# Kernel tuning notes

Measured on AMD Instinct MI355X. Metric: run time of the kernel, lower is better.

Reference implementation:

```python
import jax, jax.numpy as jnp
import numpy as np

EMBED_DIM = 1024
NUM_HEADS = 16
HEAD_DIM = EMBED_DIM // NUM_HEADS
B, S = 4, 1024
EPS = 1e-5
NEG = -1e9


def layer_norm(h, gamma, beta):
    mu = jnp.mean(h, axis=-1, keepdims=True)
    var = jnp.mean(jnp.square(h - mu), axis=-1, keepdims=True)
    return (h - mu) * jax.lax.rsqrt(var + EPS) * gamma + beta


def setup_inputs() -> dict:
    key = jax.random.key(0)
    ks = jax.random.split(key, 8)
    scale = 1.0 / np.sqrt(EMBED_DIM)
    x = jax.random.normal(ks[0], (B, S, EMBED_DIM), dtype=jnp.float32)
    mask = jax.random.randint(ks[1], (B, S, S), 0, 2).astype(jnp.bool_)
    Wq = jax.random.uniform(ks[2], (EMBED_DIM, EMBED_DIM), jnp.float32, -scale, scale)
    bq = jax.random.uniform(ks[3], (EMBED_DIM,), jnp.float32, -scale, scale)
    Wk = jax.random.uniform(ks[4], (EMBED_DIM, EMBED_DIM), jnp.float32, -scale, scale)
    bk = jax.random.uniform(ks[5], (EMBED_DIM,), jnp.float32, -scale, scale)
    gq = jnp.ones((EMBED_DIM,), jnp.float32)
    bq_n = jnp.zeros((EMBED_DIM,), jnp.float32)
    gk = jnp.ones((EMBED_DIM,), jnp.float32)
    bk_n = jnp.zeros((EMBED_DIM,), jnp.float32)
    return {"x": x, "mask": mask, "Wq": Wq, "bq": bq, "Wk": Wk, "bk": bk,
            "gq": gq, "bq_n": bq_n, "gk": gk, "bk_n": bk_n}


def reference(x, mask, Wq, bq, Wk, bk, gq, bq_n, gk, bk_n):
    b, s, _ = x.shape
    # proj -> LayerNorm -> ReLU, split heads: [B,S,H,D]
    Q = jax.nn.relu(layer_norm(x @ Wq + bq, gq, bq_n)).reshape(b, s, NUM_HEADS, HEAD_DIM)
    K = jax.nn.relu(layer_norm(x @ Wk + bk, gk, bk_n)).reshape(b, s, NUM_HEADS, HEAD_DIM)
    # scores [B,H,S,S]
    scores = jnp.einsum('bqhd,bkhd->bhqk', Q, K) / np.sqrt(HEAD_DIM).astype(np.float32)
    # symmetric masking: mask applied along keys, then (via transpose trick) along queries
    m = (mask | jnp.swapaxes(mask, -1, -2))[:, None, :, :]
    scores = jnp.where(m, NEG, scores)
    attn = jax.nn.softmax(scores, axis=-1)
    return attn.mean(axis=1)  # [B,S,S]
```

## Files before the change

kernel.cpp:

```cpp
#include <hip/hip_runtime.h>
#include <hip/hip_bf16.h>

#define B_ 4
#define S_ 1024
#define E_ 1024
#define H_ 16
#define D_ 64

typedef __attribute__((ext_vector_type(8))) short short8;
typedef __attribute__((ext_vector_type(4))) float f32x4;

static __device__ __forceinline__ unsigned short f2bf(float x) {
  unsigned int u = __float_as_uint(x);
  unsigned int r = u + 0x7fffu + ((u >> 16) & 1u);
  return (unsigned short)(r >> 16);
}
static __device__ __forceinline__ float bf2f(unsigned short b) {
  return __uint_as_float((unsigned int)b << 16);
}

#define GL2LDS16(g, l)                                                            \
  __builtin_amdgcn_global_load_lds(                                               \
      (const __attribute__((address_space(1))) unsigned int*)(g),                 \
      (__attribute__((address_space(3))) unsigned int*)(l), 16, 0, 0)

__global__ __launch_bounds__(256) void prep_kernel(const int* __restrict__ mask,
                                                   const float* __restrict__ x,
                                                   const float* __restrict__ Wq,
                                                   const float* __restrict__ Wk,
                                                   unsigned char* __restrict__ msym,
                                                   unsigned short* __restrict__ xbf,
                                                   unsigned short* __restrict__ Wt) {
  __shared__ __align__(16) char u_lds[32 * 33 * 4];
  const int blk = blockIdx.x;
  const int tid = threadIdx.x;
  if (blk < 4096) {
    int (*T)[33] = (int(*)[33])u_lds;
    const int b = blk >> 10;
    const int rest = blk & 1023;
    const int i0 = (rest >> 5) << 5;
    const int j0 = (rest & 31) << 5;
    const int ii = tid >> 3;
    const int jj4 = (tid & 7) << 2;
    const size_t bO = (size_t)b * S_ * S_;
    const int4 m2 = *(const int4*)&mask[bO + (size_t)(j0 + ii) * S_ + i0 + jj4];
    T[ii][jj4 + 0] = m2.x; T[ii][jj4 + 1] = m2.y; T[ii][jj4 + 2] = m2.z; T[ii][jj4 + 3] = m2.w;
    __syncthreads();
    const int4 m1 = *(const int4*)&mask[bO + (size_t)(i0 + ii) * S_ + j0 + jj4];
    uchar4 o;
    o.x = ((m1.x != 0) || (T[jj4 + 0][ii] != 0)) ? 1 : 0;
    o.y = ((m1.y != 0) || (T[jj4 + 1][ii] != 0)) ? 1 : 0;
    o.z = ((m1.z != 0) || (T[jj4 + 2][ii] != 0)) ? 1 : 0;
    o.w = ((m1.w != 0) || (T[jj4 + 3][ii] != 0)) ? 1 : 0;
    *(uchar4*)&msym[bO + (size_t)(i0 + ii) * S_ + j0 + jj4] = o;
  } else if (blk < 6144) {
    const size_t i = ((size_t)(blk - 4096) * 256 + tid) * 8;
    const float4 a = *(const float4*)(x + i);
    const float4 b = *(const float4*)(x + i + 4);
    const ushort4 p0 = {f2bf(a.x), f2bf(a.y), f2bf(a.z), f2bf(a.w)};
    const ushort4 p1 = {f2bf(b.x), f2bf(b.y), f2bf(b.z), f2bf(b.w)};
    *(ushort4*)(xbf + i) = p0;
    *(ushort4*)(xbf + i + 4) = p1;
  } else {
    unsigned short (*T2)[36] = (unsigned short(*)[36])u_lds;
    const int wblk = blk - 6144;
    const int mat = wblk >> 10;
    const int kt = (wblk >> 5) & 31, ntb = wblk & 31;
    const float* W = mat ? Wk : Wq;
    const int r = tid >> 3, c4 = (tid & 7) << 2;
    const float4 v = *(const float4*)&W[(size_t)(kt * 32 + r) * 1024 + ntb * 32 + c4];
    T2[r][c4 + 0] = f2bf(v.x); T2[r][c4 + 1] = f2bf(v.y);
    T2[r][c4 + 2] = f2bf(v.z); T2[r][c4 + 3] = f2bf(v.w);
    __syncthreads();
    const ushort4 o = {T2[c4 + 0][r], T2[c4 + 1][r], T2[c4 + 2][r], T2[c4 + 3][r]};
    *(ushort4*)&Wt[(size_t)(mat * 1024 + ntb * 32 + r) * 1024 + kt * 32 + c4] = o;
  }
}

__global__ __launch_bounds__(256) void gemm_mfma_kernel(const unsigned short* __restrict__ Abf,
                                                        const unsigned short* __restrict__ Wt,
                                                        unsigned short* __restrict__ P,
                                                        int nstride) {
  __shared__ __align__(16) unsigned short As[128 * 64];
  __shared__ __align__(16) unsigned short Bs[128 * 64];
  const int tid = threadIdx.x;
  const int m0 = (blockIdx.x & 31) << 7;
  const int n0 = (blockIdx.x >> 5) << 7;
  const int wave = tid >> 6, lane = tid & 63;
  const int ln15 = lane & 15, rg = lane >> 4;
  const int wm = (wave & 1) << 6;
  const int wn = (wave >> 1) << 6;
  const int sr = tid >> 3;
  const int sc = (tid & 7) << 3;
  const unsigned short* gA = Abf + (size_t)(m0 + sr) * 1024 + sc;
  const unsigned short* gB = Wt + (size_t)(n0 + sr) * 1024 + sc;
  unsigned short* lA = As + tid * 8;
  unsigned short* lB = Bs + tid * 8;
  f32x4 acc[4][4];
#pragma unroll
  for (int i = 0; i < 4; ++i)
#pragma unroll
    for (int j = 0; j < 4; ++j) acc[i][j] = (f32x4){0.0f, 0.0f, 0.0f, 0.0f};

  const unsigned short* pa = As + (wm + ln15) * 64 + rg * 8;
  const unsigned short* pb = Bs + (wn + ln15) * 64 + rg * 8;
  for (int k0 = 0; k0 < E_; k0 += 64) {
#pragma unroll
    for (int j = 0; j < 4; ++j) {
      GL2LDS16(gA + k0 + (size_t)(j * 32) * 1024, lA + j * 2048);
      GL2LDS16(gB + k0 + (size_t)(j * 32) * 1024, lB + j * 2048);
    }
    __syncthreads();
#pragma unroll
    for (int kk = 0; kk < 2; ++kk) {
      short8 af[4], bfr[4];
#pragma unroll
      for (int i = 0; i < 4; ++i) af[i] = *(const short8*)(pa + i * 16 * 64 + kk * 32);
#pragma unroll
      for (int j = 0; j < 4; ++j) bfr[j] = *(const short8*)(pb + j * 16 * 64 + kk * 32);
#pragma unroll
      for (int i = 0; i < 4; ++i)
#pragma unroll
        for (int j = 0; j < 4; ++j)
          acc[i][j] = __builtin_amdgcn_mfma_f32_16x16x32_bf16(af[i], bfr[j], acc[i][j], 0, 0, 0);
    }
    __syncthreads();
  }
#pragma unroll
  for (int i = 0; i < 4; ++i)
#pragma unroll
    for (int j = 0; j < 4; ++j)
#pragma unroll
      for (int r = 0; r < 4; ++r) {
        const int row = m0 + wm + i * 16 + rg * 4 + r;
        const int col = n0 + wn + j * 16 + ln15;
        P[(size_t)row * nstride + col] = f2bf(acc[i][j][r]);
      }
}

__global__ __launch_bounds__(256) void ln_relu_bf_kernel(const unsigned short* __restrict__ P,
                                                         int rowstride, int coloff,
                                                         const float* __restrict__ bias,
                                                         const float* __restrict__ gamma,
                                                         const float* __restrict__ beta,
                                                         unsigned short* __restrict__ obf) {
  const int row = blockIdx.x;
  const int b = row >> 10, s = row & 1023;
  const unsigned short* p = P + (size_t)row * rowstride + coloff;
  const int tid = threadIdx.x;
  const ushort4 pv = *(const ushort4*)(p + tid * 4);
  float4 v = {bf2f(pv.x), bf2f(pv.y), bf2f(pv.z), bf2f(pv.w)};
  const float4 bb = ((const float4*)bias)[tid];
  v.x += bb.x; v.y += bb.y; v.z += bb.z; v.w += bb.w;
  float sum = v.x + v.y + v.z + v.w;
  float s2 = v.x * v.x + v.y * v.y + v.z * v.z + v.w * v.w;
#pragma unroll
  for (int off = 32; off >= 1; off >>= 1) {
    sum += __shfl_xor(sum, off);
    s2 += __shfl_xor(s2, off);
  }
  __shared__ float red[2][4];
  const int wave = tid >> 6, lane = tid & 63;
  if (lane == 0) { red[0][wave] = sum; red[1][wave] = s2; }
  __syncthreads();
  sum = red[0][0] + red[0][1] + red[0][2] + red[0][3];
  s2 = red[1][0] + red[1][1] + red[1][2] + red[1][3];
  const float mu = sum * (1.0f / E_);
  const float var = s2 * (1.0f / E_) - mu * mu;
  const float r = rsqrtf(var + 1e-5f);
  const float4 g = ((const float4*)gamma)[tid];
  const float4 bt = ((const float4*)beta)[tid];
  const float o0 = fmaxf((v.x - mu) * r * g.x + bt.x, 0.0f);
  const float o1 = fmaxf((v.y - mu) * r * g.y + bt.y, 0.0f);
  const float o2 = fmaxf((v.z - mu) * r * g.z + bt.z, 0.0f);
  const float o3 = fmaxf((v.w - mu) * r * g.w + bt.w, 0.0f);
  const int h = tid >> 4;
  const int d = (tid & 15) << 2;
  const ushort4 ob = {f2bf(o0), f2bf(o1), f2bf(o2), f2bf(o3)};
  *(ushort4*)&obf[((size_t)(b * H_ + h) * S_ + s) * D_ + d] = ob;
}

__global__ __launch_bounds__(1024, 4) void attn5_kernel(const unsigned short* __restrict__ Qbf,
                                                        const unsigned short* __restrict__ Kbf,
                                                        const unsigned char* __restrict__ msym,
                                                        float* __restrict__ out) {
  __shared__ __align__(16) unsigned short Qs[256 * 64];
  __shared__ __align__(16) unsigned short Ks[2][256 * 64];
  __shared__ __align__(16) float l_lds[16][16];
  __shared__ __align__(16) float linv[16];
  const int tid = threadIdx.x;
  const int wave = tid >> 6, lane = tid & 63;
  const int ln15 = lane & 15, rg = lane >> 4;
  const int b = blockIdx.x & 3;
  const int q0 = (blockIdx.x >> 2) << 4;

  const unsigned short* Kb = Kbf + (size_t)b * H_ * S_ * D_;

  {
    const int rho = tid >> 3, p = tid & 7;
    const int c = p ^ (rho & 7);
    const int rho2 = rho + 128;
    const int c2 = p ^ (rho2 & 7);
    const uint4 v0 = *(const uint4*)(Qbf + ((size_t)(b * H_ + (rho >> 4)) * S_ + q0 + (rho & 15)) * D_ + c * 8);
    const uint4 v1 = *(const uint4*)(Qbf + ((size_t)(b * H_ + (rho2 >> 4)) * S_ + q0 + (rho2 & 15)) * D_ + c2 * 8);
    *(uint4*)&Qs[rho * 64 + p * 8] = v0;
    *(uint4*)&Qs[rho2 * 64 + p * 8] = v1;
  }
  unsigned int mbits = 0;
#pragma unroll
  for (int qt = 0; qt < 4; ++qt)
#pragma unroll
    for (int r = 0; r < 4; ++r)
      mbits |= (msym[((size_t)b * S_ + q0 + rg * 4 + r) * S_ + qt * 256 + wave * 16 + ln15] ? 1u : 0u)
               << (qt * 4 + r);

  const int krow = tid >> 3, kp = tid & 7;
  const int kcc = kp ^ (krow & 7);
  {
    const unsigned short* src = Kb + (size_t)krow * D_ + kcc * 8;
    const uint4 p0 = *(const uint4*)src;
    const uint4 p1 = *(const uint4*)(src + 128 * D_);
    *(uint4*)&Ks[0][krow * 64 + kp * 8] = p0;
    *(uint4*)&Ks[0][(krow + 128) * 64 + kp * 8] = p1;
  }
  __syncthreads();

  const int pfrag = (rg ^ (ln15 & 7)) * 8;
  const unsigned short* QsW = Qs + ln15 * 64;
  const unsigned short* KsW0 = Ks[0] + (wave * 16 + ln15) * 64;
  const unsigned short* KsW1 = Ks[1] + (wave * 16 + ln15) * 64;

  float o[4][4] = {};
  float ef[4][4];
  uint4 pf0, pf1;

#pragma unroll 1
  for (int h = 0; h < 16; ++h) {
    const unsigned short* qrow = QsW + h * 16 * 64;
    const short8 a0 = *(const short8*)(qrow + pfrag);
    const short8 a1 = *(const short8*)(qrow + (pfrag ^ 32));
    float la[4] = {0.0f, 0.0f, 0.0f, 0.0f};
#pragma unroll
    for (int qt = 0; qt < 4; ++qt) {
      const int s = h * 4 + qt;
      if (s < 63) {
        const int s1 = s + 1;
        const unsigned short* src =
            Kb + ((size_t)(s1 >> 2) * S_ + ((s1 & 3) << 8) + krow) * D_ + kcc * 8;
        pf0 = *(const uint4*)src;
        pf1 = *(const uint4*)(src + 128 * D_);
      }
      const unsigned short* kw = (qt & 1) ? KsW1 : KsW0;
      const short8 b0 = *(const short8*)(kw + pfrag);
      const short8 b1 = *(const short8*)(kw + (pfrag ^ 32));
      f32x4 cc = {0.0f, 0.0f, 0.0f, 0.0f};
      cc = __builtin_amdgcn_mfma_f32_16x16x32_bf16(a0, b0, cc, 0, 0, 0);
      cc = __builtin_amdgcn_mfma_f32_16x16x32_bf16(a1, b1, cc, 0, 0, 0);
#pragma unroll
      for (int r = 0; r < 4; ++r) {
        const float sv = fminf(cc[r] * 0.125f, 80.0f);
        const float ev = ((mbits >> (qt * 4 + r)) & 1u) ? 0.0f : __expf(sv);
        ef[qt][r] = ev;
        la[r] += ev;
      }
      if (s < 63) {
        unsigned short* dst = (qt & 1) ? Ks[0] : Ks[1];
        *(uint4*)&dst[krow * 64 + kp * 8] = pf0;
        *(uint4*)&dst[(krow + 128) * 64 + kp * 8] = pf1;
      }
      if (qt < 3) __syncthreads();
    }
#pragma unroll
    for (int r = 0; r < 4; ++r) {
      float lv = la[r];
      lv += __shfl_xor(lv, 1);
      lv += __shfl_xor(lv, 2);
      lv += __shfl_xor(lv, 4);
      lv += __shfl_xor(lv, 8);
      la[r] = lv;
    }
    if (ln15 == 0) *(float4*)&l_lds[wave][rg * 4] = (float4){la[0], la[1], la[2], la[3]};
    __syncthreads();
    if (tid < 16) {
      float ssum = 0.0f;
#pragma unroll
      for (int w = 0; w < 16; ++w) ssum += l_lds[w][tid];
      linv[tid] = 0.0625f / ssum;
    }
    __syncthreads();
    const float4 li4 = *(const float4*)&linv[rg * 4];
#pragma unroll
    for (int qt = 0; qt < 4; ++qt) {
      o[qt][0] += ef[qt][0] * li4.x;
      o[qt][1] += ef[qt][1] * li4.y;
      o[qt][2] += ef[qt][2] * li4.z;
      o[qt][3] += ef[qt][3] * li4.w;
    }
  }
#pragma unroll
  for (int qt = 0; qt < 4; ++qt)
#pragma unroll
    for (int r = 0; r < 4; ++r)
      out[((size_t)b * S_ + q0 + rg * 4 + r) * S_ + qt * 256 + wave * 16 + ln15] = o[qt][r];
}

extern "C" void kernel_launch(void* const* d_in, const int* in_sizes, int n_in,
                              void* d_out, int out_size, void* d_ws, size_t ws_size,
                              hipStream_t stream) {
  const float* x = (const float*)d_in[0];
  const int* mask = (const int*)d_in[1];
  const float* Wq = (const float*)d_in[2];
  const float* bq = (const float*)d_in[3];
  const float* Wk = (const float*)d_in[4];
  const float* bk = (const float*)d_in[5];
  const float* gq = (const float*)d_in[6];
  const float* bq_n = (const float*)d_in[7];
  const float* gk = (const float*)d_in[8];
  const float* bk_n = (const float*)d_in[9];
  float* out = (float*)d_out;

  char* ws = (char*)d_ws;
  const size_t MB = 1024 * 1024;

  if (ws_size >= 40 * MB) {
    unsigned short* P2 = (unsigned short*)ws;
    unsigned short* xbf = (unsigned short*)(ws + 16 * MB);
    unsigned short* Kbf = (unsigned short*)(ws + 16 * MB);
    unsigned short* Wt = (unsigned short*)(ws + 24 * MB);
    unsigned short* Qbf = (unsigned short*)(ws + 28 * MB);
    unsigned char* msym = (unsigned char*)(ws + 36 * MB);

    prep_kernel<<<8192, 256, 0, stream>>>(mask, x, Wq, Wk, msym, xbf, Wt);
    gemm_mfma_kernel<<<512, 256, 0, stream>>>(xbf, Wt, P2, 2048);
    ln_relu_bf_kernel<<<4096, 256, 0, stream>>>(P2, 2048, 0, bq, gq, bq_n, Qbf);
    ln_relu_bf_kernel<<<4096, 256, 0, stream>>>(P2, 2048, 1024, bk, gk, bk_n, Kbf);
    attn5_kernel<<<256, 1024, 0, stream>>>(Qbf, Kbf, msym, out);
  } else {
    unsigned short* P = (unsigned short*)ws;
    unsigned short* xbf = (unsigned short*)(ws + 8 * MB);
    unsigned short* Kbf = (unsigned short*)(ws + 8 * MB);
    unsigned short* Wt = (unsigned short*)(ws + 16 * MB);
    unsigned short* Qbf = (unsigned short*)(ws + 20 * MB);
    unsigned char* msym = (unsigned char*)(ws + 28 * MB);

    prep_kernel<<<8192, 256, 0, stream>>>(mask, x, Wq, Wk, msym, xbf, Wt);
    gemm_mfma_kernel<<<256, 256, 0, stream>>>(xbf, Wt, P, 1024);
    ln_relu_bf_kernel<<<4096, 256, 0, stream>>>(P, 1024, 0, bq, gq, bq_n, Qbf);
    gemm_mfma_kernel<<<256, 256, 0, stream>>>(xbf, Wt + (size_t)1024 * 1024, P, 1024);
    ln_relu_bf_kernel<<<4096, 256, 0, stream>>>(P, 1024, 0, bk, gk, bk_n, Kbf);
    attn5_kernel<<<256, 1024, 0, stream>>>(Qbf, Kbf, msym, out);
  }
}
```

Before: 199.1 us.

## Stream K tiles via direct global-to-LDS loads in larger halves, merge LN launches

The attention kernel now copies K tiles straight from global memory into LDS (global_load_lds) in 512-key halves instead of 256-key quarters staged through registers. This cuts the barriers per head from four to two and removes register staging. Q fragments are read directly from global memory rather than staged in LDS, and the two LayerNorm launches are merged into one 8192-block kernel. LDS use grows to two 64 KB buffers, which may reduce occupancy.

```diff
diff --git a/kernel.cpp b/kernel.cpp
--- a/kernel.cpp
+++ b/kernel.cpp
@@ -138,16 +138,9 @@
       }
 }
 
-__global__ __launch_bounds__(256) void ln_relu_bf_kernel(const unsigned short* __restrict__ P,
-                                                         int rowstride, int coloff,
-                                                         const float* __restrict__ bias,
-                                                         const float* __restrict__ gamma,
-                                                         const float* __restrict__ beta,
-                                                         unsigned short* __restrict__ obf) {
-  const int row = blockIdx.x;
-  const int b = row >> 10, s = row & 1023;
-  const unsigned short* p = P + (size_t)row * rowstride + coloff;
-  const int tid = threadIdx.x;
+__device__ __forceinline__ void ln_body(const unsigned short* p, const float* bias,
+                                        const float* gamma, const float* beta,
+                                        unsigned short* obf, int b, int s, int tid) {
   const ushort4 pv = *(const ushort4*)(p + tid * 4);
   float4 v = {bf2f(pv.x), bf2f(pv.y), bf2f(pv.z), bf2f(pv.w)};
   const float4 bb = ((const float4*)bias)[tid];
@@ -180,12 +173,39 @@
   *(ushort4*)&obf[((size_t)(b * H_ + h) * S_ + s) * D_ + d] = ob;
 }
 
-__global__ __launch_bounds__(1024, 4) void attn5_kernel(const unsigned short* __restrict__ Qbf,
+__global__ __launch_bounds__(256) void ln_relu_bf_kernel(const unsigned short* __restrict__ P,
+                                                         int rowstride, int coloff,
+                                                         const float* __restrict__ bias,
+                                                         const float* __restrict__ gamma,
+                                                         const float* __restrict__ beta,
+                                                         unsigned short* __restrict__ obf) {
+  const int row = blockIdx.x;
+  ln_body(P + (size_t)row * rowstride + coloff, bias, gamma, beta, obf,
+          row >> 10, row & 1023, threadIdx.x);
+}
+
+__global__ __launch_bounds__(256) void ln2_kernel(const unsigned short* __restrict__ P2,
+                                                  const float* __restrict__ bq,
+                                                  const float* __restrict__ gq,
+                                                  const float* __restrict__ bqn,
+                                                  const float* __restrict__ bk,
+                                                  const float* __restrict__ gk,
+                                                  const float* __restrict__ bkn,
+                                                  unsigned short* __restrict__ Qbf,
+                                                  unsigned short* __restrict__ Kbf) {
+  const int blk = blockIdx.x;
+  const int sel = blk >> 12;
+  const int row = blk & 4095;
+  ln_body(P2 + (size_t)row * 2048 + sel * 1024,
+          sel ? bk : bq, sel ? gk : gq, sel ? bkn : bqn,
+          sel ? Kbf : Qbf, row >> 10, row & 1023, threadIdx.x);
+}
+
+__global__ __launch_bounds__(1024, 4) void attn8_kernel(const unsigned short* __restrict__ Qbf,
                                                         const unsigned short* __restrict__ Kbf,
                                                         const unsigned char* __restrict__ msym,
                                                         float* __restrict__ out) {
-  __shared__ __align__(16) unsigned short Qs[256 * 64];
-  __shared__ __align__(16) unsigned short Ks[2][256 * 64];
+  __shared__ __align__(16) unsigned short Ks[2][512 * 64];
   __shared__ __align__(16) float l_lds[16][16];
   __shared__ __align__(16) float linv[16];
   const int tid = threadIdx.x;
@@ -193,115 +213,107 @@
   const int ln15 = lane & 15, rg = lane >> 4;
   const int b = blockIdx.x & 3;
   const int q0 = (blockIdx.x >> 2) << 4;
-
   const unsigned short* Kb = Kbf + (size_t)b * H_ * S_ * D_;
-
-  {
-    const int rho = tid >> 3, p = tid & 7;
-    const int c = p ^ (rho & 7);
-    const int rho2 = rho + 128;
-    const int c2 = p ^ (rho2 & 7);
-    const uint4 v0 = *(const uint4*)(Qbf + ((size_t)(b * H_ + (rho >> 4)) * S_ + q0 + (rho & 15)) * D_ + c * 8);
-    const uint4 v1 = *(const uint4*)(Qbf + ((size_t)(b * H_ + (rho2 >> 4)) * S_ + q0 + (rho2 & 15)) * D_ + c2 * 8);
-    *(uint4*)&Qs[rho * 64 + p * 8] = v0;
-    *(uint4*)&Qs[rho2 * 64 + p * 8] = v1;
-  }
+  const unsigned short* Qb = Qbf + (size_t)b * H_ * S_ * D_;
+
   unsigned int mbits = 0;
 #pragma unroll
-  for (int qt = 0; qt < 4; ++qt)
-#pragma unroll
-    for (int r = 0; r < 4; ++r)
-      mbits |= (msym[((size_t)b * S_ + q0 + rg * 4 + r) * S_ + qt * 256 + wave * 16 + ln15] ? 1u : 0u)
-               << (qt * 4 + r);
-
-  const int krow = tid >> 3, kp = tid & 7;
-  const int kcc = kp ^ (krow & 7);
-  {
-    const unsigned short* src = Kb + (size_t)krow * D_ + kcc * 8;
-    const uint4 p0 = *(const uint4*)src;
-    const uint4 p1 = *(const uint4*)(src + 128 * D_);
-    *(uint4*)&Ks[0][krow * 64 + kp * 8] = p0;
-    *(uint4*)&Ks[0][(krow + 128) * 64 + kp * 8] = p1;
-  }
+  for (int half = 0; half < 2; ++half)
+#pragma unroll
+    for (int jt = 0; jt < 2; ++jt)
+#pragma unroll
+      for (int r = 0; r < 4; ++r)
+        mbits |= (msym[((size_t)b * S_ + q0 + rg * 4 + r) * S_ + half * 512 + wave * 32 + jt * 16 + ln15]
+                      ? 1u : 0u) << (half * 8 + jt * 4 + r);
+
+  const int skey = tid >> 3;
+  const int sgc = ((tid & 7) ^ (skey & 7)) << 3;
+#pragma unroll
+  for (int c = 0; c < 4; ++c)
+    GL2LDS16(Kb + (size_t)(c * 128 + skey) * D_ + sgc, Ks[0] + c * 8192 + tid * 8);
   __syncthreads();
 
   const int pfrag = (rg ^ (ln15 & 7)) * 8;
-  const unsigned short* QsW = Qs + ln15 * 64;
-  const unsigned short* KsW0 = Ks[0] + (wave * 16 + ln15) * 64;
-  const unsigned short* KsW1 = Ks[1] + (wave * 16 + ln15) * 64;
-
-  float o[4][4] = {};
-  float ef[4][4];
-  uint4 pf0, pf1;
+  float o[2][2][4] = {};
+  float ef[2][2][4];
+  float la[4];
 
 #pragma unroll 1
   for (int h = 0; h < 16; ++h) {
-    const unsigned short* qrow = QsW + h * 16 * 64;
-    const short8 a0 = *(const short8*)(qrow + pfrag);
-    const short8 a1 = *(const short8*)(qrow + (pfrag ^ 32));
-    float la[4] = {0.0f, 0.0f, 0.0f, 0.0f};
-#pragma unroll
-    for (int qt = 0; qt < 4; ++qt) {
-      const int s = h * 4 + qt;
-      if (s < 63) {
-        const int s1 = s + 1;
-        const unsigned short* src =
-            Kb + ((size_t)(s1 >> 2) * S_ + ((s1 & 3) << 8) + krow) * D_ + kcc * 8;
-        pf0 = *(const uint4*)src;
-        pf1 = *(const uint4*)(src + 128 * D_);
+    const unsigned short* qrow = Qb + ((size_t)h * S_ + q0 + ln15) * D_ + rg * 8;
+    const short8 a0 = *(const short8*)qrow;
+    const short8 a1 = *(const short8*)(qrow + 32);
+    la[0] = la[1] = la[2] = la[3] = 0.0f;
+#pragma unroll
+    for (int half = 0; half < 2; ++half) {
+      const int s = h * 2 + half;
+      if (s < 31) {
+        const int h1 = (s + 1) >> 1, hf1 = (s + 1) & 1;
+        const unsigned short* g = Kb + (size_t)h1 * (S_ * D_) + (size_t)(hf1 * 512 + skey) * D_ + sgc;
+        unsigned short* lp = Ks[(s + 1) & 1] + tid * 8;
+#pragma unroll
+        for (int c = 0; c < 4; ++c)
+          GL2LDS16(g + (size_t)(c * 128) * D_, lp + c * 8192);
       }
-      const unsigned short* kw = (qt & 1) ? KsW1 : KsW0;
-      const short8 b0 = *(const short8*)(kw + pfrag);
-      const short8 b1 = *(const short8*)(kw + (pfrag ^ 32));
-      f32x4 cc = {0.0f, 0.0f, 0.0f, 0.0f};
-      cc = __builtin_amdgcn_mfma_f32_16x16x32_bf16(a0, b0, cc, 0, 0, 0);
-      cc = __builtin_amdgcn_mfma_f32_16x16x32_bf16(a1, b1, cc, 0, 0, 0);
-#pragma unroll
-      for (int r = 0; r < 4; ++r) {
-        const float sv = fminf(cc[r] * 0.125f, 80.0f);
-        const float ev = ((mbits >> (qt * 4 + r)) & 1u) ? 0.0f : __expf(sv);
-        ef[qt][r] = ev;
-        la[r] += ev;
+      const unsigned short* kw = Ks[s & 1] + (wave * 32 + ln15) * 64;
+#pragma unroll
+      for (int jt = 0; jt < 2; ++jt) {
+        const unsigned short* kp = kw + jt * 16 * 64;
+        const short8 b0 = *(const short8*)(kp + pfrag);
+        const short8 b1 = *(const short8*)(kp + (pfrag ^ 32));
+        f32x4 cc = {0.0f, 0.0f, 0.0f, 0.0f};
+        cc = __builtin_amdgcn_mfma_f32_16x16x32_bf16(a0, b0, cc, 0, 0, 0);
+        cc = __builtin_amdgcn_mfma_f32_16x16x32_bf16(a1, b1, cc, 0, 0, 0);
+#pragma unroll
+        for (int r = 0; r < 4; ++r) {
+          const float sv = fminf(cc[r] * 0.125f, 80.0f);
+          const float ev = ((mbits >> (half * 8 + jt * 4 + r)) & 1u) ? 0.0f : __expf(sv);
+          ef[half][jt][r] = ev;
+          la[r] += ev;
+        }
       }
-      if (s < 63) {
-        unsigned short* dst = (qt & 1) ? Ks[0] : Ks[1];
-        *(uint4*)&dst[krow * 64 + kp * 8] = pf0;
-        *(uint4*)&dst[(krow + 128) * 64 + kp * 8] = pf1;
+      if (half == 0) {
+        __syncthreads();
+      } else {
+#pragma unroll
+        for (int r = 0; r < 4; ++r) {
+          float lv = la[r];
+          lv += __shfl_xor(lv, 1);
+          lv += __shfl_xor(lv, 2);
+          lv += __shfl_xor(lv, 4);
+          lv += __shfl_xor(lv, 8);
+          la[r] = lv;
+        }
+        if (ln15 == 0) *(float4*)&l_lds[wave][rg * 4] = (float4){la[0], la[1], la[2], la[3]};
+        __syncthreads();
+        if (tid < 16) {
+          float ssum = 0.0f;
+#pragma unroll
+          for (int w = 0; w < 16; ++w) ssum += l_lds[w][tid];
+          linv[tid] = 0.0625f / ssum;
+        }
+        __syncthreads();
+        const float4 li4 = *(const float4*)&linv[rg * 4];
+#pragma unroll
+        for (int hf = 0; hf < 2; ++hf)
+#pragma unroll
+          for (int jt = 0; jt < 2; ++jt) {
+            o[hf][jt][0] += ef[hf][jt][0] * li4.x;
+            o[hf][jt][1] += ef[hf][jt][1] * li4.y;
+            o[hf][jt][2] += ef[hf][jt][2] * li4.z;
+            o[hf][jt][3] += ef[hf][jt][3] * li4.w;
+          }
       }
-      if (qt < 3) __syncthreads();
     }
-#pragma unroll
-    for (int r = 0; r < 4; ++r) {
-      float lv = la[r];
-      lv += __shfl_xor(lv, 1);
-      lv += __shfl_xor(lv, 2);
-      lv += __shfl_xor(lv, 4);
-      lv += __shfl_xor(lv, 8);
-      la[r] = lv;
-    }
-    if (ln15 == 0) *(float4*)&l_lds[wave][rg * 4] = (float4){la[0], la[1], la[2], la[3]};
-    __syncthreads();
-    if (tid < 16) {
-      float ssum = 0.0f;
-#pragma unroll
-      for (int w = 0; w < 16; ++w) ssum += l_lds[w][tid];
-      linv[tid] = 0.0625f / ssum;
-    }
-    __syncthreads();
-    const float4 li4 = *(const float4*)&linv[rg * 4];
-#pragma unroll
-    for (int qt = 0; qt < 4; ++qt) {
-      o[qt][0] += ef[qt][0] * li4.x;
-      o[qt][1] += ef[qt][1] * li4.y;
-      o[qt][2] += ef[qt][2] * li4.z;
-      o[qt][3] += ef[qt][3] * li4.w;
-    }
-  }
-#pragma unroll
-  for (int qt = 0; qt < 4; ++qt)
-#pragma unroll
-    for (int r = 0; r < 4; ++r)
-      out[((size_t)b * S_ + q0 + rg * 4 + r) * S_ + qt * 256 + wave * 16 + ln15] = o[qt][r];
+  }
+#pragma unroll
+  for (int half = 0; half < 2; ++half)
+#pragma unroll
+    for (int jt = 0; jt < 2; ++jt)
+#pragma unroll
+      for (int r = 0; r < 4; ++r)
+        out[((size_t)b * S_ + q0 + rg * 4 + r) * S_ + half * 512 + wave * 32 + jt * 16 + ln15] =
+            o[half][jt][r];
 }
 
 extern "C" void kernel_launch(void* const* d_in, const int* in_sizes, int n_in,
@@ -332,9 +344,8 @@
 
     prep_kernel<<<8192, 256, 0, stream>>>(mask, x, Wq, Wk, msym, xbf, Wt);
     gemm_mfma_kernel<<<512, 256, 0, stream>>>(xbf, Wt, P2, 2048);
-    ln_relu_bf_kernel<<<4096, 256, 0, stream>>>(P2, 2048, 0, bq, gq, bq_n, Qbf);
-    ln_relu_bf_kernel<<<4096, 256, 0, stream>>>(P2, 2048, 1024, bk, gk, bk_n, Kbf);
-    attn5_kernel<<<256, 1024, 0, stream>>>(Qbf, Kbf, msym, out);
+    ln2_kernel<<<8192, 256, 0, stream>>>(P2, bq, gq, bq_n, bk, gk, bk_n, Qbf, Kbf);
+    attn8_kernel<<<256, 1024, 0, stream>>>(Qbf, Kbf, msym, out);
   } else {
     unsigned short* P = (unsigned short*)ws;
     unsigned short* xbf = (unsigned short*)(ws + 8 * MB);
@@ -348,6 +359,6 @@
     ln_relu_bf_kernel<<<4096, 256, 0, stream>>>(P, 1024, 0, bq, gq, bq_n, Qbf);
     gemm_mfma_kernel<<<256, 256, 0, stream>>>(xbf, Wt + (size_t)1024 * 1024, P, 1024);
     ln_relu_bf_kernel<<<4096, 256, 0, stream>>>(P, 1024, 0, bk, gk, bk_n, Kbf);
-    attn5_kernel<<<256, 1024, 0, stream>>>(Qbf, Kbf, msym, out);
-  }
-}
+    attn8_kernel<<<256, 1024, 0, stream>>>(Qbf, Kbf, msym, out);
+  }
+}
```

New measurement: 197.2 us. About the same (-0.9%).
